# Kernel tuning notes

Hardware: AMD Instinct MI355X
Metric: run time of the kernel (lower is better)

The kernel has to match this reference:

```python
import jax, jax.numpy as jnp
import numpy as np

D_MODEL = 1024
NUM_HEADS = 16
D_HEAD = D_MODEL // NUM_HEADS
MAX_LEN = 16384
BATCH = 4
SEQ = 1024


def setup_inputs() -> dict:
    key = jax.random.key(0)
    ks = jax.random.split(key, 10)
    s = 1.0 / np.sqrt(D_MODEL)
    return {
        "q_in": jax.random.normal(ks[0], (BATCH, SEQ, D_MODEL), jnp.float32),
        "k_in": jax.random.normal(ks[1], (BATCH, SEQ, D_MODEL), jnp.float32),
        "v_in": jax.random.normal(ks[2], (BATCH, SEQ, D_MODEL), jnp.float32),
        "Wq": jax.random.normal(ks[3], (D_MODEL, D_MODEL), jnp.float32) * s,
        "bq": jnp.zeros((D_MODEL,), jnp.float32),
        "Wk": jax.random.normal(ks[4], (D_MODEL, D_MODEL), jnp.float32) * s,
        "bk": jnp.zeros((D_MODEL,), jnp.float32),
        "Wv": jax.random.normal(ks[5], (D_MODEL, D_MODEL), jnp.float32) * s,
        "bv": jnp.zeros((D_MODEL,), jnp.float32),
        "Er": jax.random.normal(ks[6], (MAX_LEN, D_HEAD), jnp.float32),
    }


def _skew(QEr):
    # QEr: [B, H, S, S] -> pad one zero column on the left, reshape, drop row 0
    B, H, S, _ = QEr.shape
    padded = jnp.pad(QEr, ((0, 0), (0, 0), (0, 0), (1, 0)))  # [B,H,S,S+1]
    reshaped = padded.reshape(B, H, S + 1, S)
    return reshaped[:, :, 1:, :]  # [B,H,S,S]


def reference(q_in, k_in, v_in, Wq, bq, Wk, bk, Wv, bv, Er):
    B, S, _ = q_in.shape
    H, Dh = NUM_HEADS, D_HEAD
    # projections, split into heads: [B, H, S, Dh]
    q = (q_in @ Wq + bq).reshape(B, S, H, Dh).transpose(0, 2, 1, 3)
    k = (k_in @ Wk + bk).reshape(B, S, H, Dh).transpose(0, 2, 1, 3)
    v = (v_in @ Wv + bv).reshape(B, S, H, Dh).transpose(0, 2, 1, 3)
    # relative position scores: Er slice [S, Dh]
    Er_sl = Er[MAX_LEN - S:, :]
    QEr = jnp.einsum('bhsd,td->bhst', q, Er_sl)  # [B,H,S,S]
    Srel = _skew(QEr)
    QK = jnp.einsum('bhsd,bhtd->bhst', q, k)
    attn = (QK + Srel) / jnp.sqrt(jnp.asarray(Dh, q.dtype))
    attn = jax.nn.softmax(attn, axis=-1)
    out = jnp.einsum('bhst,bhtd->bhsd', attn, v)  # [B,H,S,Dh]
    out = out.transpose(0, 2, 1, 3).reshape(B, S, H * Dh)
    return out
```

## Files before the change

### kernel.cpp

```cpp
#include <hip/hip_runtime.h>
#include <hip/hip_bf16.h>
#include <cstdint>

#define S_LEN 1024
#define DMODEL 1024
#define NHEADS 16
#define DHEAD 64
#define MAXLEN 16384
#define BATCH 4

typedef __attribute__((ext_vector_type(8))) short bf16x8;
typedef __attribute__((ext_vector_type(4))) float f32x4;

#define AS1(p) ((const __attribute__((address_space(1))) unsigned int*)(p))
#define AS3(p) ((__attribute__((address_space(3))) unsigned int*)(p))

__device__ inline unsigned short f2b(float f) {
  unsigned int u = __float_as_uint(f);
  unsigned int r = (u + 0x7FFFu + ((u >> 16) & 1u)) >> 16;
  return (unsigned short)r;
}
__device__ inline float b2f(unsigned short u) {
  return __uint_as_float(((unsigned int)u) << 16);
}

#define LDSWZ(row, slot) (((row) << 6) + (((slot) ^ ((row) & 7)) << 3))

__global__ __launch_bounds__(256) void convert_all(
    const float* __restrict__ W0, const float* __restrict__ W1, const float* __restrict__ W2,
    unsigned short* __restrict__ T0, unsigned short* __restrict__ T1, unsigned short* __restrict__ T2,
    const float* __restrict__ Er, unsigned short* __restrict__ Erb,
    const float* __restrict__ X0, const float* __restrict__ X1, const float* __restrict__ X2,
    unsigned short* __restrict__ B0, unsigned short* __restrict__ B1, unsigned short* __restrict__ B2) {
  const int z = blockIdx.z;
  if (z >= 4) {
    const float* X = (z == 4) ? X0 : (z == 5) ? X1 : X2;
    unsigned short* B = (z == 4) ? B0 : (z == 5) ? B1 : B2;
    size_t i = (((size_t)blockIdx.y * 32 + blockIdx.x) * 256 + threadIdx.x) * 16;
    union { unsigned short hh[16]; int4 v[2]; } u;
#pragma unroll
    for (int r = 0; r < 4; ++r) {
      float4 f = *(const float4*)(X + i + r * 4);
      u.hh[r * 4 + 0] = f2b(f.x); u.hh[r * 4 + 1] = f2b(f.y);
      u.hh[r * 4 + 2] = f2b(f.z); u.hh[r * 4 + 3] = f2b(f.w);
    }
    *(int4*)(B + i) = u.v[0];
    *(int4*)(B + i + 8) = u.v[1];
    return;
  }
  if (z == 3) {
    const int o = blockIdx.y * 32 + blockIdx.x;
    if (o < 64) {
      const int i = o * 1024 + threadIdx.x * 4;
      float4 f = *(const float4*)(Er + (size_t)(MAXLEN - S_LEN) * DHEAD + i);
      Erb[i] = f2b(f.x); Erb[i + 1] = f2b(f.y);
      Erb[i + 2] = f2b(f.z); Erb[i + 3] = f2b(f.w);
    }
    return;
  }
  const float* W = (z == 0) ? W0 : (z == 1) ? W1 : W2;
  unsigned short* WT = (z == 0) ? T0 : (z == 1) ? T1 : T2;
  __shared__ float t[32][33];
  const int bi = blockIdx.y * 32, bj = blockIdx.x * 32;
  const int r = threadIdx.x >> 3, c4 = (threadIdx.x & 7) * 4;
  float4 f = *(const float4*)&W[(size_t)(bi + r) * DMODEL + bj + c4];
  t[r][c4] = f.x; t[r][c4 + 1] = f.y; t[r][c4 + 2] = f.z; t[r][c4 + 3] = f.w;
  __syncthreads();
  ushort4 u;
  u.x = f2b(t[c4][r]); u.y = f2b(t[c4 + 1][r]);
  u.z = f2b(t[c4 + 2][r]); u.w = f2b(t[c4 + 3][r]);
  *(ushort4*)&WT[(size_t)(bj + r) * DMODEL + bi + c4] = u;
}

__global__ __launch_bounds__(256) void proj_glds3(
    const unsigned short* __restrict__ Xq, const unsigned short* __restrict__ Xk,
    const unsigned short* __restrict__ Xv,
    const unsigned short* __restrict__ T0, const unsigned short* __restrict__ T1,
    const unsigned short* __restrict__ T2,
    const float* __restrict__ b0, const float* __restrict__ b1, const float* __restrict__ b2,
    unsigned short* __restrict__ O0, unsigned short* __restrict__ O1,
    unsigned short* __restrict__ O2) {
  const int z = blockIdx.z;
  const unsigned short* X = (z == 0) ? Xq : (z == 1) ? Xk : Xv;
  const unsigned short* WT = (z == 0) ? T0 : (z == 1) ? T1 : T2;
  const float* bias = (z == 0) ? b0 : (z == 1) ? b1 : b2;
  unsigned short* Out = (z == 0) ? O0 : (z == 1) ? O1 : O2;
  const float osc = (z == 0) ? 0.125f : 1.0f;
  __shared__ unsigned short As[128 * 64];
  __shared__ unsigned short Bs[128 * 64];
  const int tid = threadIdx.x;
  const int l = tid & 63, w = tid >> 6;
  const int o = blockIdx.y * 8 + blockIdx.x;
  const int lid = (o & 7) * 32 + (o >> 3);
  const int bm = (lid >> 3) * 128, bn = (lid & 7) * 128;
  const int wr = (w >> 1) * 64, wc = (w & 1) * 64;
  const int lrow = l >> 3;
  const int slotlog = (l & 7) ^ (lrow & 7);
  const unsigned short* Xa = X + (size_t)(bm + lrow) * DMODEL + slotlog * 8;
  const unsigned short* Wa = WT + (size_t)(bn + lrow) * DMODEL + slotlog * 8;
  f32x4 acc[4][4] = {};
  for (int k0 = 0; k0 < DMODEL; k0 += 64) {
    __syncthreads();
#pragma unroll
    for (int j = 0; j < 4; ++j) {
      int r8 = (w * 4 + j) * 8;
      __builtin_amdgcn_global_load_lds(AS1(Xa + (size_t)r8 * DMODEL + k0),
                                       AS3(&As[(w * 4 + j) * 512]), 16, 0, 0);
      __builtin_amdgcn_global_load_lds(AS1(Wa + (size_t)r8 * DMODEL + k0),
                                       AS3(&Bs[(w * 4 + j) * 512]), 16, 0, 0);
    }
    __syncthreads();
#pragma unroll
    for (int ks = 0; ks < 2; ++ks) {
      bf16x8 a[4], b[4];
#pragma unroll
      for (int f = 0; f < 4; ++f) {
        int row = wr + f * 16 + (l & 15);
        a[f] = *(const bf16x8*)&As[LDSWZ(row, ks * 4 + (l >> 4))];
        int col = wc + f * 16 + (l & 15);
        b[f] = *(const bf16x8*)&Bs[LDSWZ(col, ks * 4 + (l >> 4))];
      }
#pragma unroll
      for (int i = 0; i < 4; ++i)
#pragma unroll
        for (int j = 0; j < 4; ++j)
          acc[i][j] = __builtin_amdgcn_mfma_f32_16x16x32_bf16(a[i], b[j], acc[i][j], 0, 0, 0);
    }
  }
#pragma unroll
  for (int i = 0; i < 4; ++i) {
    int m = bm + wr + i * 16 + ((l >> 4) << 2);
#pragma unroll
    for (int j = 0; j < 4; ++j) {
      int n = bn + wc + j * 16 + (l & 15);
      float bv = bias[n];
#pragma unroll
      for (int e = 0; e < 4; ++e)
        Out[(size_t)(m + e) * DMODEL + n] = f2b((acc[i][j][e] + bv) * osc);
    }
  }
}

__global__ __launch_bounds__(256) void qer_mfma(const unsigned short* __restrict__ qp,
    const unsigned short* __restrict__ Erb, unsigned short* __restrict__ G, int bh0) {
  const int bh = bh0 + blockIdx.z;
  const int b = bh >> 4, h = bh & 15;
  __shared__ unsigned short As[128 * 64];
  __shared__ unsigned short Bs[128 * 64];
  const int tid = threadIdx.x, l = tid & 63, wid = tid >> 6;
  const int bm = blockIdx.y * 128, bn = blockIdx.x * 128;
  const int wr = (wid >> 1) * 64, wc = (wid & 1) * 64;
  const unsigned short* qb = qp + (size_t)b * S_LEN * DMODEL + h * DHEAD;
  unsigned short* Gc = G + (size_t)blockIdx.z * S_LEN * S_LEN;
#pragma unroll
  for (int r = 0; r < 4; ++r) {
    int s = r * 256 + tid;
    int row = s >> 3, sl = s & 7;
    *(int4*)&As[LDSWZ(row, sl)] = *(const int4*)(qb + (size_t)(bm + row) * DMODEL + sl * 8);
    *(int4*)&Bs[LDSWZ(row, sl)] = *(const int4*)(Erb + (size_t)(bn + row) * DHEAD + sl * 8);
  }
  if (blockIdx.x == 0 && tid < 128) {
    int s = bm + tid;
    if (s < S_LEN - 1) Gc[(size_t)s * S_LEN + s + 1] = 0;
  }
  __syncthreads();
  f32x4 acc[4][4] = {};
#pragma unroll
  for (int ks = 0; ks < 2; ++ks) {
    bf16x8 a[4], b[4];
#pragma unroll
    for (int f = 0; f < 4; ++f) {
      int row = wr + f * 16 + (l & 15);
      a[f] = *(const bf16x8*)&As[LDSWZ(row, ks * 4 + (l >> 4))];
      int col = wc + f * 16 + (l & 15);
      b[f] = *(const bf16x8*)&Bs[LDSWZ(col, ks * 4 + (l >> 4))];
    }
#pragma unroll
    for (int i = 0; i < 4; ++i)
#pragma unroll
      for (int j = 0; j < 4; ++j)
        acc[i][j] = __builtin_amdgcn_mfma_f32_16x16x32_bf16(a[i], b[j], acc[i][j], 0, 0, 0);
  }
#pragma unroll
  for (int i = 0; i < 4; ++i) {
    int m = bm + wr + i * 16 + ((l >> 4) << 2);
#pragma unroll
    for (int j = 0; j < 4; ++j) {
      int n = bn + wc + j * 16 + (l & 15);
      int base = 1025 * m + n - 1023;
#pragma unroll
      for (int e = 0; e < 4; ++e) {
        int addr = base + 1025 * e;
        if (addr >= 0)
          Gc[addr] = f2b(acc[i][j][e]);
      }
    }
  }
}

__global__ __launch_bounds__(256) void attn_skew(const unsigned short* __restrict__ qp,
    const unsigned short* __restrict__ kp, const unsigned short* __restrict__ vp,
    const unsigned short* __restrict__ G, float* __restrict__ out, int bh0, int nb) {
  const int o = blockIdx.y * 16 + blockIdx.x;
  const int q8 = nb * 2;
  const int lid = (o & 7) * q8 + (o >> 3);
  const int s0 = (lid & 15) * 64;
  const int bhl = lid >> 4;
  const int bh = bh0 + bhl;
  const int b = bh >> 4, h = bh & 15;
  __shared__ unsigned short Qs[64 * 64];
  __shared__ unsigned short Ks[64 * 64];
  __shared__ unsigned short Vt[64 * 64];
  __shared__ unsigned short Ps[4][16 * 64];
  const int tid = threadIdx.x, l = tid & 63, w = tid >> 6;
  const int lg = l >> 4, li = l & 15;
  const unsigned short* qb = qp + (size_t)b * S_LEN * DMODEL + h * DHEAD;
  const unsigned short* kb = kp + (size_t)b * S_LEN * DMODEL + h * DHEAD;
  const unsigned short* vb = vp + (size_t)b * S_LEN * DMODEL + h * DHEAD;
  const unsigned short* Gb = G + (size_t)bhl * S_LEN * S_LEN;

#pragma unroll
  for (int r = 0; r < 2; ++r) {
    int s = r * 256 + tid;
    int row = s >> 3, sl = s & 7;
    *(int4*)&Qs[LDSWZ(row, sl)] = *(const int4*)(qb + (size_t)(s0 + row) * DMODEL + sl * 8);
  }
  __syncthreads();
  bf16x8 qf[2];
#pragma unroll
  for (int ks = 0; ks < 2; ++ks)
    qf[ks] = *(const bf16x8*)&Qs[LDSWZ(w * 16 + li, ks * 4 + lg)];

  const int lrow = l >> 3;
  const int chk = (l & 7) ^ lrow;
  const unsigned short* Ka = kb + (size_t)(w * 8 + lrow) * DMODEL + chk * 8;

  f32x4 o4[4] = {};
  float lsum[4] = {0.f, 0.f, 0.f, 0.f};
  int sg[4];
  const unsigned short* gp[4];
#pragma unroll
  for (int i = 0; i < 4; ++i) {
    sg[i] = s0 + w * 16 + (lg << 2) + i;
    gp[i] = Gb + (size_t)sg[i] * S_LEN + li;
  }
  const int pr = tid & 31, dh0 = (tid >> 5) * 8;
  const float L2E = 1.44269504f;
  const float SHF = 16.f * 1.44269504f;

  for (int ti = 0; ti < 16; ++ti) {
    const int t0 = ti * 64;
    __syncthreads();
    __builtin_amdgcn_global_load_lds(AS1(Ka + (size_t)t0 * DMODEL),
                                     AS3(&Ks[(w * 64) * 8]), 16, 0, 0);
    __builtin_amdgcn_global_load_lds(AS1(Ka + (size_t)(t0 + 32) * DMODEL),
                                     AS3(&Ks[(256 + w * 64) * 8]), 16, 0, 0);
    {
      const unsigned short* v0p = vb + (size_t)(t0 + pr * 2) * DMODEL + dh0;
      union { int4 v; unsigned short hh[8]; } va, vc;
      va.v = *(const int4*)v0p;
      vc.v = *(const int4*)(v0p + DMODEL);
      unsigned int* vtw = (unsigned int*)Vt;
#pragma unroll
      for (int j = 0; j < 8; ++j) {
        int dh = dh0 + j;
        int widx = dh * 32 + (((pr >> 2) ^ (dh & 7)) << 2) + (pr & 3);
        vtw[widx] = (unsigned int)va.hh[j] | ((unsigned int)vc.hh[j] << 16);
      }
    }
    __syncthreads();
    unsigned short rv[4][4];
#pragma unroll
    for (int f = 0; f < 4; ++f)
#pragma unroll
      for (int i = 0; i < 4; ++i)
        rv[f][i] = gp[i][t0 + f * 16];
    f32x4 sa[4] = {};
#pragma unroll
    for (int ks = 0; ks < 2; ++ks)
#pragma unroll
      for (int f = 0; f < 4; ++f) {
        bf16x8 kf = *(const bf16x8*)&Ks[LDSWZ(f * 16 + li, ks * 4 + lg)];
        sa[f] = __builtin_amdgcn_mfma_f32_16x16x32_bf16(qf[ks], kf, sa[f], 0, 0, 0);
      }
    unsigned short* Pw = &Ps[w][0];
#pragma unroll
    for (int f = 0; f < 4; ++f) {
#pragma unroll
      for (int i = 0; i < 4; ++i) {
        float sv = sa[f][i] + b2f(rv[f][i]);
        float pv = __builtin_exp2f(__builtin_fmaf(sv, L2E, -SHF));
        unsigned int pu = __float_as_uint(pv) & 0xffff0000u;
        lsum[i] += __uint_as_float(pu);
        int prow = (lg << 2) + i, pcol = f * 16 + li;
        Pw[LDSWZ(prow, pcol >> 3) + (pcol & 7)] = (unsigned short)(pu >> 16);
      }
    }
#pragma unroll
    for (int ks = 0; ks < 2; ++ks) {
      bf16x8 pf = *(const bf16x8*)&Pw[LDSWZ(li, ks * 4 + lg)];
#pragma unroll
      for (int f = 0; f < 4; ++f) {
        bf16x8 vf = *(const bf16x8*)&Vt[LDSWZ(f * 16 + li, ks * 4 + lg)];
        o4[f] = __builtin_amdgcn_mfma_f32_16x16x32_bf16(pf, vf, o4[f], 0, 0, 0);
      }
    }
  }
#pragma unroll
  for (int off = 8; off >= 1; off >>= 1)
#pragma unroll
    for (int i = 0; i < 4; ++i) lsum[i] += __shfl_xor(lsum[i], off);
#pragma unroll
  for (int i = 0; i < 4; ++i) {
    float inv = 1.f / lsum[i];
#pragma unroll
    for (int f = 0; f < 4; ++f)
      out[(size_t)(b * S_LEN + sg[i]) * DMODEL + h * DHEAD + f * 16 + li] = o4[f][i] * inv;
  }
}

extern "C" void kernel_launch(void* const* d_in, const int* in_sizes, int n_in,
                              void* d_out, int out_size, void* d_ws, size_t ws_size,
                              hipStream_t stream) {
  (void)in_sizes; (void)n_in; (void)out_size;
  const float* q_in = (const float*)d_in[0];
  const float* k_in = (const float*)d_in[1];
  const float* v_in = (const float*)d_in[2];
  const float* Wq   = (const float*)d_in[3];
  const float* bq   = (const float*)d_in[4];
  const float* Wk   = (const float*)d_in[5];
  const float* bk   = (const float*)d_in[6];
  const float* Wv   = (const float*)d_in[7];
  const float* bv   = (const float*)d_in[8];
  const float* Er   = (const float*)d_in[9];
  float* out = (float*)d_out;

  char* ws = (char*)d_ws;
  const size_t MB = (size_t)1 << 20;
  unsigned short* wtq = (unsigned short*)(ws);
  unsigned short* wtk = (unsigned short*)(ws + 2 * MB);
  unsigned short* wtv = (unsigned short*)(ws + 4 * MB);
  unsigned short* erb = (unsigned short*)(ws + 6 * MB);
  unsigned short* qp  = (unsigned short*)(ws + 8 * MB);
  unsigned short* kp  = (unsigned short*)(ws + 16 * MB);
  unsigned short* vp  = (unsigned short*)(ws + 24 * MB);
  unsigned short* xq  = (unsigned short*)(ws + 32 * MB);
  unsigned short* xk  = (unsigned short*)(ws + 40 * MB);
  unsigned short* xv  = (unsigned short*)(ws + 48 * MB);
  unsigned short* G   = (unsigned short*)(ws + 56 * MB);

  const size_t gavail = (ws_size > 56 * MB) ? (ws_size - 56 * MB) : 0;
  int chunk = (int)(gavail / (2 * MB));
  if (chunk < 1) chunk = 1;
  if (chunk > 64) chunk = 64;

  dim3 blk(256);
  hipLaunchKernelGGL(convert_all, dim3(32, 32, 7), blk, 0, stream,
                     Wq, Wk, Wv, wtq, wtk, wtv, Er, erb,
                     q_in, k_in, v_in, xq, xk, xv);

  dim3 gproj(DMODEL / 128, (BATCH * S_LEN) / 128, 3);
  hipLaunchKernelGGL(proj_glds3, gproj, blk, 0, stream,
                     xq, xk, xv, wtq, wtk, wtv, bq, bk, bv, qp, kp, vp);

  for (int bh0 = 0; bh0 < BATCH * NHEADS; bh0 += chunk) {
    int nb = BATCH * NHEADS - bh0;
    if (nb > chunk) nb = chunk;
    dim3 gqer(S_LEN / 128, S_LEN / 128, nb);
    hipLaunchKernelGGL(qer_mfma, gqer, blk, 0, stream, qp, erb, G, bh0);
    dim3 gattn(16, nb);
    hipLaunchKernelGGL(attn_skew, gattn, blk, 0, stream, qp, kp, vp, G, out, bh0, nb);
  }
}
```

Measured before the change: 153.4 us.

## Pre-transpose V into per-head layout and async-load it into LDS

Adds a separate kernel that transposes each head's V projection into a [bh, dh, t] buffer. The attention kernel then loads V tiles directly into LDS with global_load_lds, using the same XOR swizzle as the K loads. This replaces the per-iteration register gather and eight scalar LDS writes per thread. The cost is an extra kernel launch, an extra 8 MB round trip through memory, and 8 MB more workspace, which reduces the space left for the G chunk buffer.

After: 155.9 us. Within noise of the previous version (+1.6%).

```diff
diff --git a/kernel.cpp b/kernel.cpp
--- a/kernel.cpp
+++ b/kernel.cpp
@@ -141,6 +141,33 @@
   }
 }
 
+__global__ __launch_bounds__(256) void vt_transpose(const unsigned short* __restrict__ vp,
+                                                    unsigned short* __restrict__ vtp) {
+  const int bh = blockIdx.y;
+  const int b = bh >> 4, h = bh & 15;
+  const int t0 = blockIdx.x * 64;
+  __shared__ unsigned short T[64 * 72];
+  const int tid = threadIdx.x;
+  const unsigned short* src = vp + ((size_t)(b * S_LEN + t0) * DMODEL) + h * DHEAD;
+#pragma unroll
+  for (int r = 0; r < 2; ++r) {
+    int s = r * 256 + tid;
+    int row = s >> 3, c8 = s & 7;
+    *(int4*)&T[row * 72 + c8 * 8] = *(const int4*)(src + (size_t)row * DMODEL + c8 * 8);
+  }
+  __syncthreads();
+  unsigned short* dst = vtp + (size_t)bh * (DHEAD * S_LEN) + t0;
+#pragma unroll
+  for (int r = 0; r < 2; ++r) {
+    int o = r * 256 + tid;
+    int dh = o >> 3, c8 = o & 7;
+    union { unsigned short hh[8]; int4 v; } u;
+#pragma unroll
+    for (int k = 0; k < 8; ++k) u.hh[k] = T[(c8 * 8 + k) * 72 + dh];
+    *(int4*)(dst + (size_t)dh * S_LEN + c8 * 8) = u.v;
+  }
+}
+
 __global__ __launch_bounds__(256) void qer_mfma(const unsigned short* __restrict__ qp,
     const unsigned short* __restrict__ Erb, unsigned short* __restrict__ G, int bh0) {
   const int bh = bh0 + blockIdx.z;
@@ -199,7 +226,7 @@
 }
 
 __global__ __launch_bounds__(256) void attn_skew(const unsigned short* __restrict__ qp,
-    const unsigned short* __restrict__ kp, const unsigned short* __restrict__ vp,
+    const unsigned short* __restrict__ kp, const unsigned short* __restrict__ vtp,
     const unsigned short* __restrict__ G, float* __restrict__ out, int bh0, int nb) {
   const int o = blockIdx.y * 16 + blockIdx.x;
   const int q8 = nb * 2;
@@ -216,7 +243,6 @@
   const int lg = l >> 4, li = l & 15;
   const unsigned short* qb = qp + (size_t)b * S_LEN * DMODEL + h * DHEAD;
   const unsigned short* kb = kp + (size_t)b * S_LEN * DMODEL + h * DHEAD;
-  const unsigned short* vb = vp + (size_t)b * S_LEN * DMODEL + h * DHEAD;
   const unsigned short* Gb = G + (size_t)bhl * S_LEN * S_LEN;
 
 #pragma unroll
@@ -234,6 +260,8 @@
   const int lrow = l >> 3;
   const int chk = (l & 7) ^ lrow;
   const unsigned short* Ka = kb + (size_t)(w * 8 + lrow) * DMODEL + chk * 8;
+  const unsigned short* Va = vtp + (size_t)bh * (DHEAD * S_LEN)
+                               + (size_t)(w * 8 + lrow) * S_LEN + chk * 8;
 
   f32x4 o4[4] = {};
   float lsum[4] = {0.f, 0.f, 0.f, 0.f};
@@ -244,7 +272,6 @@
     sg[i] = s0 + w * 16 + (lg << 2) + i;
     gp[i] = Gb + (size_t)sg[i] * S_LEN + li;
   }
-  const int pr = tid & 31, dh0 = (tid >> 5) * 8;
   const float L2E = 1.44269504f;
   const float SHF = 16.f * 1.44269504f;
 
@@ -255,19 +282,10 @@
                                      AS3(&Ks[(w * 64) * 8]), 16, 0, 0);
     __builtin_amdgcn_global_load_lds(AS1(Ka + (size_t)(t0 + 32) * DMODEL),
                                      AS3(&Ks[(256 + w * 64) * 8]), 16, 0, 0);
-    {
-      const unsigned short* v0p = vb + (size_t)(t0 + pr * 2) * DMODEL + dh0;
-      union { int4 v; unsigned short hh[8]; } va, vc;
-      va.v = *(const int4*)v0p;
-      vc.v = *(const int4*)(v0p + DMODEL);
-      unsigned int* vtw = (unsigned int*)Vt;
-#pragma unroll
-      for (int j = 0; j < 8; ++j) {
-        int dh = dh0 + j;
-        int widx = dh * 32 + (((pr >> 2) ^ (dh & 7)) << 2) + (pr & 3);
-        vtw[widx] = (unsigned int)va.hh[j] | ((unsigned int)vc.hh[j] << 16);
-      }
-    }
+    __builtin_amdgcn_global_load_lds(AS1(Va + t0),
+                                     AS3(&Vt[(w * 64) * 8]), 16, 0, 0);
+    __builtin_amdgcn_global_load_lds(AS1(Va + 32 * S_LEN + t0),
+                                     AS3(&Vt[(256 + w * 64) * 8]), 16, 0, 0);
     __syncthreads();
     unsigned short rv[4][4];
 #pragma unroll
@@ -347,9 +365,10 @@
   unsigned short* xq  = (unsigned short*)(ws + 32 * MB);
   unsigned short* xk  = (unsigned short*)(ws + 40 * MB);
   unsigned short* xv  = (unsigned short*)(ws + 48 * MB);
-  unsigned short* G   = (unsigned short*)(ws + 56 * MB);
-
-  const size_t gavail = (ws_size > 56 * MB) ? (ws_size - 56 * MB) : 0;
+  unsigned short* vtp = (unsigned short*)(ws + 56 * MB);
+  unsigned short* G   = (unsigned short*)(ws + 64 * MB);
+
+  const size_t gavail = (ws_size > 64 * MB) ? (ws_size - 64 * MB) : 0;
   int chunk = (int)(gavail / (2 * MB));
   if (chunk < 1) chunk = 1;
   if (chunk > 64) chunk = 64;
@@ -362,6 +381,8 @@
   dim3 gproj(DMODEL / 128, (BATCH * S_LEN) / 128, 3);
   hipLaunchKernelGGL(proj_glds3, gproj, blk, 0, stream,
                      xq, xk, xv, wtq, wtk, wtv, bq, bk, bv, qp, kp, vp);
+
+  hipLaunchKernelGGL(vt_transpose, dim3(16, 64), blk, 0, stream, vp, vtp);
 
   for (int bh0 = 0; bh0 < BATCH * NHEADS; bh0 += chunk) {
     int nb = BATCH * NHEADS - bh0;
@@ -369,6 +390,6 @@
     dim3 gqer(S_LEN / 128, S_LEN / 128, nb);
     hipLaunchKernelGGL(qer_mfma, gqer, blk, 0, stream, qp, erb, G, bh0);
     dim3 gattn(16, nb);
-    hipLaunchKernelGGL(attn_skew, gattn, blk, 0, stream, qp, kp, vp, G, out, bh0, nb);
-  }
-}
+    hipLaunchKernelGGL(attn_skew, gattn, blk, 0, stream, qp, kp, vtp, G, out, bh0, nb);
+  }
+}
```
